# Optimization experiments

Hardware: AMD Instinct MI355X
Metric: run time of the kernel (lower is better)

The kernel has to match this reference:

```python
import jax, jax.numpy as jnp
import numpy as np

N_HEADS = 8
NUM_TIME_STEPS = 17  # T = NUM_TIME_STEPS - 1 = 16
MASK_PAD = np.float32(-2**32 + 1)


def setup_inputs() -> dict:
    key = jax.random.key(0)
    ks = jax.random.split(key, 5)
    B, T, D = 32768, NUM_TIME_STEPS - 1, 128
    return {
        "inputs": jax.random.normal(ks[0], (B, T, D), dtype=jnp.float32),
        "pos_emb": jax.random.normal(ks[1], (NUM_TIME_STEPS, D), dtype=jnp.float32) * 0.1,
        "Wq": jax.random.normal(ks[2], (D, D), dtype=jnp.float32) * (1.0 / np.sqrt(D)),
        "Wk": jax.random.normal(ks[3], (D, D), dtype=jnp.float32) * (1.0 / np.sqrt(D)),
        "Wv": jax.random.normal(ks[4], (D, D), dtype=jnp.float32) * (1.0 / np.sqrt(D)),
    }


def reference(inputs, pos_emb, Wq, Wk, Wv):
    B, T, D = inputs.shape
    h = N_HEADS
    dh = Wq.shape[1] // h
    # add positional embeddings for the first T time steps
    x = inputs + pos_emb[:T][None, :, :]  # [B, T, D]
    # QKV projections, then split into heads (torch.split dim=2 + cat dim=0 == head-major [h, B, T, dh])
    def proj(W):
        return jnp.einsum("btd,de->bte", x, W).reshape(B, T, h, dh).transpose(2, 0, 1, 3)
    q, k, v = proj(Wq), proj(Wk), proj(Wv)  # each [h, B, T, dh]
    # scaled scores; NOTE: original scales by sqrt(num_time_steps), not sqrt(head_dim)
    scores = jnp.einsum("hbtd,hbsd->hbts", q, k) / jnp.float32(NUM_TIME_STEPS) ** 0.5
    # causal mask: masked positions set to -2**32+1 (finite pad, as in the original)
    causal = jnp.tril(jnp.ones((T, T), dtype=bool))
    scores = jnp.where(causal[None, None, :, :], scores, MASK_PAD)
    attn = jax.nn.softmax(scores, axis=-1)  # [h, B, T, T]
    o = jnp.einsum("hbts,hbsd->hbtd", attn, v)  # [h, B, T, dh]
    # re-concat heads along feature dim (split dim0 + cat dim2)
    o = o.transpose(1, 2, 0, 3).reshape(B, T, h * dh)
    # feedforward: relu(x) + x
    o = jax.nn.relu(o) + o
    # residual=True: concat with temporal (position-added) inputs along features
    return jnp.concatenate([o, x], axis=2)  # [B, T, output_dim + input_dim]
```

## Files before the change

kernel.cpp:

```cpp
#include <hip/hip_runtime.h>

typedef float    f32x4 __attribute__((ext_vector_type(4)));
typedef __bf16   bf16x8 __attribute__((ext_vector_type(8)));
typedef _Float16 f16x4 __attribute__((ext_vector_type(4)));

typedef __attribute__((address_space(1))) const void gas_void;
typedef __attribute__((address_space(3))) void las_void;

static __device__ __forceinline__ unsigned short f2bf(float f) {
  union { float f; unsigned int u; } a; a.f = f;
  unsigned int r = (a.u + 0x7FFFu + ((a.u >> 16) & 1u)) >> 16;
  return (unsigned short)r;
}

#define QSCALE_L2E 0.34992146f

__global__ void prep_weights(const float* __restrict__ Wq, const float* __restrict__ Wk,
                             const float* __restrict__ Wv, unsigned short* __restrict__ wf) {
  int idx = blockIdx.x * 256 + threadIdx.x;
  if (idx >= 3 * 8 * 4 * 64 * 8) return;
  int i  = idx & 7;
  int p  = (idx >> 3) & 63;
  int kk = (idx >> 9) & 3;
  int n  = (idx >> 11) & 7;
  int w  = idx >> 14;
  const float* W = (w == 0) ? Wq : ((w == 1) ? Wk : Wv);
  float val = W[(kk * 32 + (p >> 4) * 8 + i) * 128 + n * 16 + (p & 15)];
  if (w == 0) val *= QSCALE_L2E;
  wf[idx] = f2bf(val);
}

__global__ void prep_posw(const float* __restrict__ pos, const float* __restrict__ Wq,
                          const float* __restrict__ Wk, const float* __restrict__ Wv,
                          float* __restrict__ pw) {
  int idx = blockIdx.x * 256 + threadIdx.x;
  if (idx >= 3 * 8 * 64 * 4) return;
  int r = idx & 3;
  int l = (idx >> 2) & 63;
  int h = (idx >> 8) & 7;
  int w = idx >> 11;
  const float* W = (w == 0) ? Wq : ((w == 1) ? Wk : Wv);
  int t, d;
  if (w < 2) { t = l & 15;            d = h * 16 + (l >> 4) * 4 + r; }
  else       { t = (l >> 4) * 4 + r;  d = h * 16 + (l & 15); }
  float s = 0.f;
  for (int k = 0; k < 128; ++k) s += pos[t * 128 + k] * W[k * 128 + d];
  if (w == 0) s *= QSCALE_L2E;
  pw[idx] = s;
}

__global__ void __launch_bounds__(256, 2)
attn_main(const float* __restrict__ xin, const float* __restrict__ pos,
          const unsigned short* __restrict__ wfrag, const float* __restrict__ pw,
          float* __restrict__ out, int B) {
  __shared__ __align__(16) float lx[2][4][2048];

  const int tid   = threadIdx.x;
  const int wid   = tid >> 6;
  const int l     = tid & 63;
  const int frow  = l & 15;
  const int fkq   = l >> 4;
  const int trow0 = fkq * 4;
  const int n0    = wid * 2;

  bf16x8 wf[3][2][4];
#pragma unroll
  for (int w = 0; w < 3; ++w)
#pragma unroll
    for (int hl = 0; hl < 2; ++hl)
#pragma unroll
      for (int kk = 0; kk < 4; ++kk)
        wf[w][hl][kk] = *(const bf16x8*)(wfrag + ((w * 32 + (n0 + hl) * 4 + kk) * 512) + l * 8);

  f32x4 posw[3][2];
#pragma unroll
  for (int w = 0; w < 3; ++w)
#pragma unroll
    for (int hl = 0; hl < 2; ++hl)
      posw[w][hl] = *(const f32x4*)(pw + ((w * 8 + n0 + hl) * 64 + l) * 4);

  const int ptc = wid * 32 + fkq * 8;
  const f32x4 pp0 = *(const f32x4*)(pos + frow * 128 + ptc);
  const f32x4 pp1 = *(const f32x4*)(pos + frow * 128 + ptc + 4);

  const f32x4 zero4 = {0.f, 0.f, 0.f, 0.f};

  const int bpi   = gridDim.x * 4;
  const int niter = B / bpi;
  const int gsb   = frow * 128 + fkq * 8;

  {
    const float* xb = xin + (size_t)(blockIdx.x * 4 + wid) * 2048;
#pragma unroll
    for (int c = 0; c < 8; ++c)
      __builtin_amdgcn_global_load_lds((gas_void*)(xb + gsb + (c >> 1) * 32 + (c & 1) * 4),
                                       (las_void*)&lx[0][wid][c * 256], 16, 0, 0);
  }
  int buf = 0;

  for (int it = 0; it < niter; ++it) {
    const int b0 = blockIdx.x * 4 + it * bpi;

    if (it == 0) {
      __syncthreads();
    } else {
      asm volatile("s_waitcnt vmcnt(16)" ::: "memory");
      __builtin_amdgcn_s_barrier();
    }

    if (it + 1 < niter) {
      const float* xb2 = xin + (size_t)(b0 + bpi + wid) * 2048;
#pragma unroll
      for (int c = 0; c < 8; ++c)
        __builtin_amdgcn_global_load_lds((gas_void*)(xb2 + gsb + (c >> 1) * 32 + (c & 1) * 4),
                                         (las_void*)&lx[buf ^ 1][wid][c * 256], 16, 0, 0);
    }
    asm volatile("" ::: "memory");

#pragma unroll
    for (int g = 0; g < 4; ++g) {
      const float* lb = &lx[buf][g][0];
      float* ob = out + (size_t)(b0 + g) * 4096;

      bf16x8 xf[4];
#pragma unroll
      for (int kk = 0; kk < 4; ++kk) {
        f32x4 a0 = *(const f32x4*)(lb + (2 * kk + 0) * 256 + l * 4);
        f32x4 a1 = *(const f32x4*)(lb + (2 * kk + 1) * 256 + l * 4);
        xf[kk][0] = (__bf16)a0.x; xf[kk][1] = (__bf16)a0.y;
        xf[kk][2] = (__bf16)a0.z; xf[kk][3] = (__bf16)a0.w;
        xf[kk][4] = (__bf16)a1.x; xf[kk][5] = (__bf16)a1.y;
        xf[kk][6] = (__bf16)a1.z; xf[kk][7] = (__bf16)a1.w;
      }
      {
        f32x4 c0 = *(const f32x4*)(lb + (2 * wid + 0) * 256 + l * 4);
        f32x4 c1 = *(const f32x4*)(lb + (2 * wid + 1) * 256 + l * 4);
        *(f32x4*)(ob + frow * 256 + 128 + ptc)     = c0 + pp0;
        *(f32x4*)(ob + frow * 256 + 128 + ptc + 4) = c1 + pp1;
      }

#pragma unroll
      for (int hl = 0; hl < 2; ++hl) {
        f32x4 qa = posw[0][hl], ka = posw[1][hl], va = posw[2][hl];
#pragma unroll
        for (int kk = 0; kk < 4; ++kk) {
          qa = __builtin_amdgcn_mfma_f32_16x16x32_bf16(wf[0][hl][kk], xf[kk], qa, 0, 0, 0);
          ka = __builtin_amdgcn_mfma_f32_16x16x32_bf16(wf[1][hl][kk], xf[kk], ka, 0, 0, 0);
          va = __builtin_amdgcn_mfma_f32_16x16x32_bf16(xf[kk], wf[2][hl][kk], va, 0, 0, 0);
        }
        f16x4 qh, kh, vh;
#pragma unroll
        for (int r = 0; r < 4; ++r) {
          qh[r] = (_Float16)qa[r];
          kh[r] = (_Float16)ka[r];
          vh[r] = (_Float16)va[r];
        }

        f32x4 st = __builtin_amdgcn_mfma_f32_16x16x16f16(kh, qh, zero4, 0, 0, 0);
        float p0 = (trow0 + 0 <= frow) ? __builtin_amdgcn_exp2f(st[0]) : 0.f;
        float p1 = (trow0 + 1 <= frow) ? __builtin_amdgcn_exp2f(st[1]) : 0.f;
        float p2 = (trow0 + 2 <= frow) ? __builtin_amdgcn_exp2f(st[2]) : 0.f;
        float p3 = (trow0 + 3 <= frow) ? __builtin_amdgcn_exp2f(st[3]) : 0.f;
        float ssum = (p0 + p1) + (p2 + p3);
        ssum += __shfl_xor(ssum, 16);
        ssum += __shfl_xor(ssum, 32);
        float inv = __builtin_amdgcn_rcpf(ssum);
        f16x4 ah;
        ah[0] = (_Float16)(p0 * inv);
        ah[1] = (_Float16)(p1 * inv);
        ah[2] = (_Float16)(p2 * inv);
        ah[3] = (_Float16)(p3 * inv);

        f32x4 ot = __builtin_amdgcn_mfma_f32_16x16x16f16(vh, ah, zero4, 0, 0, 0);
        f32x4 ov;
#pragma unroll
        for (int r = 0; r < 4; ++r) {
          float x = ot[r];
          ov[r] = x > 0.f ? 2.f * x : x;
        }
        *(f32x4*)(ob + frow * 256 + (n0 + hl) * 16 + trow0) = ov;
      }
    }

    buf ^= 1;
  }
}

extern "C" void kernel_launch(void* const* d_in, const int* in_sizes, int n_in,
                              void* d_out, int out_size, void* d_ws, size_t ws_size,
                              hipStream_t stream) {
  (void)n_in; (void)out_size; (void)ws_size;
  const float* xin = (const float*)d_in[0];
  const float* pos = (const float*)d_in[1];
  const float* Wq  = (const float*)d_in[2];
  const float* Wk  = (const float*)d_in[3];
  const float* Wv  = (const float*)d_in[4];
  float* out = (float*)d_out;
  unsigned short* wf = (unsigned short*)d_ws;
  float* pw = (float*)((char*)d_ws + 3 * 8 * 4 * 64 * 8 * sizeof(unsigned short));
  int B = in_sizes[0] / 2048;

  hipLaunchKernelGGL(prep_weights, dim3(192), dim3(256), 0, stream, Wq, Wk, Wv, wf);
  hipLaunchKernelGGL(prep_posw, dim3(24), dim3(256), 0, stream, pos, Wq, Wk, Wv, pw);
  hipLaunchKernelGGL(attn_main, dim3(512), dim3(256), 0, stream, xin, pos, wf, pw, out, B);
}
```

Measured before the change: 173.0 us.

## Use 512-thread blocks with one head per wave instead of two

Doubles the block to 8 waves so each wave computes a single attention head rather than two. The per-wave weight fragments and positional projections are halved, and the async LDS prefetch of inputs is split so two waves share each batch element. Launch bounds now target 4 blocks per SM. This aims to cut register pressure and raise occupancy for better latency hiding. The cost is that each wave now re-reads and re-converts the full x fragment from LDS for only one head, doubling LDS reads and bf16 conversions per unit of work.

```diff
diff --git a/kernel.cpp b/kernel.cpp
--- a/kernel.cpp
+++ b/kernel.cpp
@@ -49,7 +49,7 @@
   pw[idx] = s;
 }
 
-__global__ void __launch_bounds__(256, 2)
+__global__ void __launch_bounds__(512, 4)
 attn_main(const float* __restrict__ xin, const float* __restrict__ pos,
           const unsigned short* __restrict__ wfrag, const float* __restrict__ pw,
           float* __restrict__ out, int B) {
@@ -61,40 +61,40 @@
   const int frow  = l & 15;
   const int fkq   = l >> 4;
   const int trow0 = fkq * 4;
-  const int n0    = wid * 2;
-
-  bf16x8 wf[3][2][4];
+
+  bf16x8 wf[3][4];
 #pragma unroll
   for (int w = 0; w < 3; ++w)
 #pragma unroll
-    for (int hl = 0; hl < 2; ++hl)
-#pragma unroll
-      for (int kk = 0; kk < 4; ++kk)
-        wf[w][hl][kk] = *(const bf16x8*)(wfrag + ((w * 32 + (n0 + hl) * 4 + kk) * 512) + l * 8);
-
-  f32x4 posw[3][2];
+    for (int kk = 0; kk < 4; ++kk)
+      wf[w][kk] = *(const bf16x8*)(wfrag + ((w * 32 + wid * 4 + kk) * 512) + l * 8);
+
+  f32x4 posw[3];
 #pragma unroll
   for (int w = 0; w < 3; ++w)
-#pragma unroll
-    for (int hl = 0; hl < 2; ++hl)
-      posw[w][hl] = *(const f32x4*)(pw + ((w * 8 + n0 + hl) * 64 + l) * 4);
-
-  const int ptc = wid * 32 + fkq * 8;
-  const f32x4 pp0 = *(const f32x4*)(pos + frow * 128 + ptc);
-  const f32x4 pp1 = *(const f32x4*)(pos + frow * 128 + ptc + 4);
+    posw[w] = *(const f32x4*)(pw + ((w * 8 + wid) * 64 + l) * 4);
+
+  const int ptcol = wid * 16 + fkq * 4;
+  const f32x4 pp = *(const f32x4*)(pos + frow * 128 + ptcol);
+  const int q    = 4 * wid + fkq;
+  const int ptIdx = (((q >> 3) << 1) | (q & 1)) * 256 + (((q & 7) >> 1) * 16 + frow) * 4;
 
   const f32x4 zero4 = {0.f, 0.f, 0.f, 0.f};
 
   const int bpi   = gridDim.x * 4;
   const int niter = B / bpi;
   const int gsb   = frow * 128 + fkq * 8;
+  const int bw    = wid >> 1;
+  const int c0    = (wid & 1) * 4;
 
   {
-    const float* xb = xin + (size_t)(blockIdx.x * 4 + wid) * 2048;
-#pragma unroll
-    for (int c = 0; c < 8; ++c)
+    const float* xb = xin + (size_t)(blockIdx.x * 4 + bw) * 2048;
+#pragma unroll
+    for (int j = 0; j < 4; ++j) {
+      int c = c0 + j;
       __builtin_amdgcn_global_load_lds((gas_void*)(xb + gsb + (c >> 1) * 32 + (c & 1) * 4),
-                                       (las_void*)&lx[0][wid][c * 256], 16, 0, 0);
+                                       (las_void*)&lx[0][bw][c * 256], 16, 0, 0);
+    }
   }
   int buf = 0;
 
@@ -104,16 +104,18 @@
     if (it == 0) {
       __syncthreads();
     } else {
-      asm volatile("s_waitcnt vmcnt(16)" ::: "memory");
+      asm volatile("s_waitcnt vmcnt(8)" ::: "memory");
       __builtin_amdgcn_s_barrier();
     }
 
     if (it + 1 < niter) {
-      const float* xb2 = xin + (size_t)(b0 + bpi + wid) * 2048;
-#pragma unroll
-      for (int c = 0; c < 8; ++c)
+      const float* xb2 = xin + (size_t)(b0 + bpi + bw) * 2048;
+#pragma unroll
+      for (int j = 0; j < 4; ++j) {
+        int c = c0 + j;
         __builtin_amdgcn_global_load_lds((gas_void*)(xb2 + gsb + (c >> 1) * 32 + (c & 1) * 4),
-                                         (las_void*)&lx[buf ^ 1][wid][c * 256], 16, 0, 0);
+                                         (las_void*)&lx[buf ^ 1][bw][c * 256], 16, 0, 0);
+      }
     }
     asm volatile("" ::: "memory");
 
@@ -133,53 +135,48 @@
         xf[kk][6] = (__bf16)a1.z; xf[kk][7] = (__bf16)a1.w;
       }
       {
-        f32x4 c0 = *(const f32x4*)(lb + (2 * wid + 0) * 256 + l * 4);
-        f32x4 c1 = *(const f32x4*)(lb + (2 * wid + 1) * 256 + l * 4);
-        *(f32x4*)(ob + frow * 256 + 128 + ptc)     = c0 + pp0;
-        *(f32x4*)(ob + frow * 256 + 128 + ptc + 4) = c1 + pp1;
-      }
-
-#pragma unroll
-      for (int hl = 0; hl < 2; ++hl) {
-        f32x4 qa = posw[0][hl], ka = posw[1][hl], va = posw[2][hl];
-#pragma unroll
-        for (int kk = 0; kk < 4; ++kk) {
-          qa = __builtin_amdgcn_mfma_f32_16x16x32_bf16(wf[0][hl][kk], xf[kk], qa, 0, 0, 0);
-          ka = __builtin_amdgcn_mfma_f32_16x16x32_bf16(wf[1][hl][kk], xf[kk], ka, 0, 0, 0);
-          va = __builtin_amdgcn_mfma_f32_16x16x32_bf16(xf[kk], wf[2][hl][kk], va, 0, 0, 0);
-        }
-        f16x4 qh, kh, vh;
-#pragma unroll
-        for (int r = 0; r < 4; ++r) {
-          qh[r] = (_Float16)qa[r];
-          kh[r] = (_Float16)ka[r];
-          vh[r] = (_Float16)va[r];
-        }
-
-        f32x4 st = __builtin_amdgcn_mfma_f32_16x16x16f16(kh, qh, zero4, 0, 0, 0);
-        float p0 = (trow0 + 0 <= frow) ? __builtin_amdgcn_exp2f(st[0]) : 0.f;
-        float p1 = (trow0 + 1 <= frow) ? __builtin_amdgcn_exp2f(st[1]) : 0.f;
-        float p2 = (trow0 + 2 <= frow) ? __builtin_amdgcn_exp2f(st[2]) : 0.f;
-        float p3 = (trow0 + 3 <= frow) ? __builtin_amdgcn_exp2f(st[3]) : 0.f;
-        float ssum = (p0 + p1) + (p2 + p3);
-        ssum += __shfl_xor(ssum, 16);
-        ssum += __shfl_xor(ssum, 32);
-        float inv = __builtin_amdgcn_rcpf(ssum);
-        f16x4 ah;
-        ah[0] = (_Float16)(p0 * inv);
-        ah[1] = (_Float16)(p1 * inv);
-        ah[2] = (_Float16)(p2 * inv);
-        ah[3] = (_Float16)(p3 * inv);
-
-        f32x4 ot = __builtin_amdgcn_mfma_f32_16x16x16f16(vh, ah, zero4, 0, 0, 0);
-        f32x4 ov;
-#pragma unroll
-        for (int r = 0; r < 4; ++r) {
-          float x = ot[r];
-          ov[r] = x > 0.f ? 2.f * x : x;
-        }
-        *(f32x4*)(ob + frow * 256 + (n0 + hl) * 16 + trow0) = ov;
-      }
+        f32x4 c0v = *(const f32x4*)(lb + ptIdx);
+        *(f32x4*)(ob + frow * 256 + 128 + ptcol) = c0v + pp;
+      }
+
+      f32x4 qa = posw[0], ka = posw[1], va = posw[2];
+#pragma unroll
+      for (int kk = 0; kk < 4; ++kk) {
+        qa = __builtin_amdgcn_mfma_f32_16x16x32_bf16(wf[0][kk], xf[kk], qa, 0, 0, 0);
+        ka = __builtin_amdgcn_mfma_f32_16x16x32_bf16(wf[1][kk], xf[kk], ka, 0, 0, 0);
+        va = __builtin_amdgcn_mfma_f32_16x16x32_bf16(xf[kk], wf[2][kk], va, 0, 0, 0);
+      }
+      f16x4 qh, kh, vh;
+#pragma unroll
+      for (int r = 0; r < 4; ++r) {
+        qh[r] = (_Float16)qa[r];
+        kh[r] = (_Float16)ka[r];
+        vh[r] = (_Float16)va[r];
+      }
+
+      f32x4 st = __builtin_amdgcn_mfma_f32_16x16x16f16(kh, qh, zero4, 0, 0, 0);
+      float p0 = (trow0 + 0 <= frow) ? __builtin_amdgcn_exp2f(st[0]) : 0.f;
+      float p1 = (trow0 + 1 <= frow) ? __builtin_amdgcn_exp2f(st[1]) : 0.f;
+      float p2 = (trow0 + 2 <= frow) ? __builtin_amdgcn_exp2f(st[2]) : 0.f;
+      float p3 = (trow0 + 3 <= frow) ? __builtin_amdgcn_exp2f(st[3]) : 0.f;
+      float ssum = (p0 + p1) + (p2 + p3);
+      ssum += __shfl_xor(ssum, 16);
+      ssum += __shfl_xor(ssum, 32);
+      float inv = __builtin_amdgcn_rcpf(ssum);
+      f16x4 ah;
+      ah[0] = (_Float16)(p0 * inv);
+      ah[1] = (_Float16)(p1 * inv);
+      ah[2] = (_Float16)(p2 * inv);
+      ah[3] = (_Float16)(p3 * inv);
+
+      f32x4 ot = __builtin_amdgcn_mfma_f32_16x16x16f16(vh, ah, zero4, 0, 0, 0);
+      f32x4 ov;
+#pragma unroll
+      for (int r = 0; r < 4; ++r) {
+        float x = ot[r];
+        ov[r] = x > 0.f ? 2.f * x : x;
+      }
+      *(f32x4*)(ob + frow * 256 + wid * 16 + trow0) = ov;
     }
 
     buf ^= 1;
@@ -202,5 +199,5 @@
 
   hipLaunchKernelGGL(prep_weights, dim3(192), dim3(256), 0, stream, Wq, Wk, Wv, wf);
   hipLaunchKernelGGL(prep_posw, dim3(24), dim3(256), 0, stream, pos, Wq, Wk, Wv, pw);
-  hipLaunchKernelGGL(attn_main, dim3(512), dim3(256), 0, stream, xin, pos, wf, pw, out, B);
-}
+  hipLaunchKernelGGL(attn_main, dim3(512), dim3(512), 0, stream, xin, pos, wf, pw, out, B);
+}
```

Result: no change. 176.2 us (+1.8%).
